# Performance work log

Hardware: AMD Instinct MI355X
Metric: run time of the kernel (lower is better)

## Reference

```python
import jax, jax.numpy as jnp
import numpy as np

N_NODES = 10000
N_EDGES = 640000
IN_CH, HID, OUT_CH = 128, 128, 64


def _gcn_conv(x, edge_index, edge_weight, W, b, n_nodes):
    # PyG GCNConv (default add_self_loops=True, normalize=True, bias=True):
    #   A_hat = A + I ; D = rowsum(A_hat) ; norm_e = D^-1/2[src] * w_e * D^-1/2[dst]
    #   out[dst] += norm_e * (x @ W)[src] ; out += b
    src, dst = edge_index[0], edge_index[1]
    loop = jnp.arange(n_nodes, dtype=edge_index.dtype)
    src = jnp.concatenate([src, loop])
    dst = jnp.concatenate([dst, loop])
    w = jnp.concatenate([edge_weight, jnp.ones((n_nodes,), edge_weight.dtype)])
    deg = jax.ops.segment_sum(w, dst, num_segments=n_nodes)  # scatter on col
    dinv = jnp.where(deg > 0, jax.lax.rsqrt(deg), 0.0).astype(x.dtype)
    norm = dinv[src] * w * dinv[dst]  # [E+N]
    xw = x @ W  # dense GEMM [N, out]
    msg = norm[:, None] * xw[src]  # gather + scale [E+N, out]
    out = jax.ops.segment_sum(msg, dst, num_segments=n_nodes)  # scatter-add
    return out + b


def setup_inputs() -> dict:
    key = jax.random.key(0)
    ks = jax.random.split(key, 8)
    x = jax.random.normal(ks[0], (N_NODES, IN_CH), dtype=jnp.float32)
    edge_index = jax.random.randint(ks[1], (2, N_EDGES), 0, N_NODES, dtype=jnp.int64)
    edge_weight = jax.random.uniform(ks[2], (N_EDGES,), dtype=jnp.float32)
    W1 = jax.random.normal(ks[3], (IN_CH, HID), dtype=jnp.float32) * 0.05
    b1 = jnp.zeros((HID,), jnp.float32)
    W2 = jax.random.normal(ks[4], (HID, OUT_CH), dtype=jnp.float32) * 0.05
    b2 = jnp.zeros((OUT_CH,), jnp.float32)
    return {"x": x, "edge_index": edge_index, "edge_weight": edge_weight,
            "W1": W1, "b1": b1, "W2": W2, "b2": b2}


def reference(x, edge_index, edge_weight, W1, b1, W2, b2):
    h = _gcn_conv(x, edge_index, edge_weight, W1, b1, N_NODES)
    h = jax.nn.relu(h)
    out = _gcn_conv(h, edge_index, edge_weight, W2, b2, N_NODES)
    return out
```

## Files before the change

kernel.cpp:

```cpp
#include <hip/hip_runtime.h>
#include <math.h>

#define N_NODES 10000
#define N_EDGES 640000
#define ELLW    192

#define CHUNKS  64
#define CHUNK_E 10000
#define GB      313

typedef unsigned long long ull;
typedef unsigned int uint;
typedef unsigned short ushort;
typedef unsigned char uchar;

#define FIXED_SCALE 262144.0f


__device__ __forceinline__ float bf_lo(uint u) { return __uint_as_float(u << 16); }
__device__ __forceinline__ float bf_hi(uint u) { return __uint_as_float(u & 0xffff0000u); }
__device__ __forceinline__ ushort f2bf(float v) {
    uint u = __float_as_uint(v);
    uint r = u + 0x7fffu + ((u >> 16) & 1u);
    return (ushort)(r >> 16);
}

__global__ __launch_bounds__(256) void kernelA(const int* __restrict__ ei,
                                               const float* __restrict__ ew,
                                               uint* __restrict__ sd32,
                                               uint* __restrict__ blockcnt,
                                               const float* __restrict__ x,
                                               const float* __restrict__ W1,
                                               ushort* __restrict__ xw1b) {
    __shared__ uint smem[N_NODES];
    const int tid = threadIdx.x;
    if (blockIdx.x < CHUNKS) {
        const int c = blockIdx.x;
        __shared__ int sflag;
        if (tid == 0) sflag = 0;
        for (int i = tid; i < N_NODES; i += 256) smem[i] = 0u;
        __syncthreads();
        int a = (tid < 64) ? ei[2 * (c * CHUNK_E + tid) + 1] : 0;
        if (a) atomicOr(&sflag, 1);
        __syncthreads();
        const int f = sflag;
        const ull* ei64 = (const ull*)ei;
        for (int k = tid; k < CHUNK_E; k += 256) {
            int e = c * CHUNK_E + k;
            int s, d;
            if (f) { s = ei[e];        d = ei[N_EDGES + e]; }
            else   { s = (int)ei64[e]; d = (int)ei64[N_EDGES + e]; }
            float w = ew[e];
            uint fx = (uint)(w * FIXED_SCALE + 0.5f);
            uint old = atomicAdd(&smem[d], (1u << 24) | fx);
            uint r = (old >> 24) & 15u;
            sd32[e] = (r << 28) | ((uint)d << 14) | (uint)s;
        }
        __syncthreads();
        for (int i = tid; i < N_NODES; i += 256)
            blockcnt[c * N_NODES + i] = smem[i];
    } else {
        constexpr int K = 128, TM = 32, KT = 32, NCOL = 128, RPT = 16;
        float* sA = (float*)smem;
        float* sB = sA + TM * (KT + 1);
        int blk = blockIdx.x - CHUNKS;
        int c = tid % NCOL, rr = tid / NCOL;
        int row0 = blk * TM;
        float acc[RPT];
#pragma unroll
        for (int r = 0; r < RPT; ++r) acc[r] = 0.0f;
        for (int k0 = 0; k0 < K; k0 += KT) {
            for (int i = tid; i < TM * KT; i += 256) {
                int r = i / KT, k = i % KT;
                int gr = row0 + r;
                sA[r * (KT + 1) + k] = (gr < N_NODES) ? x[gr * K + k0 + k] : 0.0f;
            }
            for (int i = tid; i < KT * NCOL; i += 256) {
                int k = i / NCOL, cc = i % NCOL;
                sB[k * NCOL + cc] = W1[(k0 + k) * NCOL + cc];
            }
            __syncthreads();
#pragma unroll
            for (int k = 0; k < KT; ++k) {
                float b = sB[k * NCOL + c];
#pragma unroll
                for (int r = 0; r < RPT; ++r)
                    acc[r] += sA[(rr * RPT + r) * (KT + 1) + k] * b;
            }
            __syncthreads();
        }
#pragma unroll
        for (int r = 0; r < RPT; ++r) {
            int gr = row0 + rr * RPT + r;
            if (gr < N_NODES) xw1b[gr * NCOL + c] = f2bf(acc[r]);
        }
    }
}

__global__ __launch_bounds__(256) void scanB(const uint* __restrict__ blockcnt,
                                             uchar* __restrict__ base8,
                                             int* __restrict__ cnt_arr,
                                             float* __restrict__ dinv) {
    int n = blockIdx.x * 256 + threadIdx.x;
    if (n >= N_NODES) return;
    uint wsum = 0;
    int run = 0;
#pragma unroll 8
    for (int c = 0; c < CHUNKS; ++c) {
        uint v = blockcnt[c * N_NODES + n];
        base8[c * N_NODES + n] = (uchar)run;
        run += (int)(v >> 24);
        wsum += v & 0xffffffu;
    }
    cnt_arr[n] = run;
    float dg = 1.0f + (float)wsum * (1.0f / FIXED_SCALE);
    dinv[n] = (float)(1.0 / sqrt((double)dg));
}

__global__ __launch_bounds__(256) void fillC(const uint* __restrict__ sd32,
                                             const float* __restrict__ ew,
                                             const uchar* __restrict__ base8,
                                             const float* __restrict__ dinv,
                                             ull* __restrict__ epack) {
    const int gid = blockIdx.x * 256 + threadIdx.x;
    const int stride = gridDim.x * 256;
    for (int e = gid; e < N_EDGES; e += stride) {
        uint sd = sd32[e];
        int s = (int)(sd & 0x3fffu);
        int d = (int)((sd >> 14) & 0x3fffu);
        int r = (int)(sd >> 28);
        int c = e / CHUNK_E;
        float nrm = dinv[s] * ew[e] * dinv[d];
        int slot = (int)base8[c * N_NODES + d] + r;
        if (slot < ELLW)
            epack[d * ELLW + slot] = ((ull)__float_as_uint(nrm) << 32) | (ull)(uint)s;
    }
}

__global__ __launch_bounds__(256) void aggC(const ushort* __restrict__ xw1b,
                                            const ull* __restrict__ epack,
                                            const int* __restrict__ cnt_arr,
                                            const float* __restrict__ dinv,
                                            const float* __restrict__ b1,
                                            const float* __restrict__ W2,
                                            ushort* __restrict__ xw2b) {
    __shared__ float hl[4][128];
    __shared__ float w2s[128 * 64];
    const uint* __restrict__ xw32 = (const uint*)xw1b;
    const int tid = threadIdx.x;
    int l = tid & 63;
    int wv = tid >> 6;
    int node = blockIdx.x * 4 + wv;

    for (int i = tid; i < 128 * 64; i += 256) w2s[i] = W2[i];

    int cnt = __builtin_amdgcn_readfirstlane(cnt_arr[node]);
    if (cnt > ELLW) cnt = ELLW;
    float dn = dinv[node];
    float d2 = dn * dn;
    uint su = xw32[node * 64 + l];
    float acc0 = d2 * bf_lo(su);
    float acc1 = d2 * bf_hi(su);
    const ull* ep = epack + (long)node * ELLW;
#pragma unroll 8
    for (int j = 0; j < cnt; ++j) {
        ull v = ep[j];
        uint s = (uint)v;
        float n = __uint_as_float((uint)(v >> 32));
        uint u = xw32[s * 64 + l];
        acc0 = fmaf(n, bf_lo(u), acc0);
        acc1 = fmaf(n, bf_hi(u), acc1);
    }
    float2 bb = ((const float2*)b1)[l];
    hl[wv][2 * l]     = fmaxf(acc0 + bb.x, 0.0f);
    hl[wv][2 * l + 1] = fmaxf(acc1 + bb.y, 0.0f);
    __syncthreads();

    float acc = 0.0f;
#pragma unroll 8
    for (int k = 0; k < 128; ++k)
        acc = fmaf(hl[wv][k], w2s[k * 64 + l], acc);
    xw2b[node * 64 + l] = f2bf(acc);
}

__global__ __launch_bounds__(256) void agg2(const ushort* __restrict__ xw2b,
                                            const ull* __restrict__ epack,
                                            const int* __restrict__ cnt_arr,
                                            const float* __restrict__ dinv,
                                            const float* __restrict__ b2,
                                            float* __restrict__ out) {
    const uint* __restrict__ xw32 = (const uint*)xw2b;
    int lane = threadIdx.x & 63;
    int half = lane >> 5;
    int q = lane & 31;
    int pair = blockIdx.x * 4 + (threadIdx.x >> 6);
    int A = pair * 2, B = A + 1;
    int cntA = __builtin_amdgcn_readfirstlane(cnt_arr[A]);
    int cntB = __builtin_amdgcn_readfirstlane(cnt_arr[B]);
    if (cntA > ELLW) cntA = ELLW;
    if (cntB > ELLW) cntB = ELLW;
    int myn = half ? B : A;
    int mycnt = half ? cntB : cntA;
    float dn = dinv[myn];
    float d2 = dn * dn;
    uint su = xw32[myn * 32 + q];
    float acc0 = d2 * bf_lo(su);
    float acc1 = d2 * bf_hi(su);
    const ull* epA = epack + (long)A * ELLW;
    const ull* epB = epack + (long)B * ELLW;
    int mx = cntA > cntB ? cntA : cntB;
#pragma unroll 4
    for (int j = 0; j < mx; ++j) {
        ull vA = epA[j];
        ull vB = epB[j];
        ull v = half ? vB : vA;
        uint s = (uint)v & 0xffffu;
        float n = (j < mycnt) ? __uint_as_float((uint)(v >> 32)) : 0.0f;
        uint u = xw32[s * 32 + q];
        acc0 = fmaf(n, bf_lo(u), acc0);
        acc1 = fmaf(n, bf_hi(u), acc1);
    }
    float2 bb = ((const float2*)b2)[q];
    float2 o;
    o.x = acc0 + bb.x;
    o.y = acc1 + bb.y;
    ((float2*)out)[myn * 32 + q] = o;
}

extern "C" void kernel_launch(void* const* d_in, const int* in_sizes, int n_in,
                              void* d_out, int out_size, void* d_ws, size_t ws_size,
                              hipStream_t stream) {
    const float* x  = (const float*)d_in[0];
    const int*   ei = (const int*)d_in[1];
    const float* ew = (const float*)d_in[2];
    const float* W1 = (const float*)d_in[3];
    const float* b1 = (const float*)d_in[4];
    const float* W2 = (const float*)d_in[5];
    const float* b2 = (const float*)d_in[6];
    float* out = (float*)d_out;

    char* ws = (char*)d_ws;
    ushort* xw1b    = (ushort*)(ws + 0);
    ushort* xw2b    = (ushort*)(ws + 5120000);
    ull*    epack   = (ull*)   (ws + 6400000);
    uint*   blockcnt= (uint*)  (ws + 21760000);
    uchar*  base8   = (uchar*) (ws + 26880000);
    uint*   sd32    = (uint*)  (ws + 28800000);
    int*    cnt_arr = (int*)   (ws + 31360000);
    float*  dinv    = (float*) (ws + 31400000);

    kernelA<<<CHUNKS + GB, 256, 0, stream>>>(ei, ew, sd32, blockcnt, x, W1, xw1b);
    scanB<<<(N_NODES + 255) / 256, 256, 0, stream>>>(blockcnt, base8, cnt_arr, dinv);
    fillC<<<512, 256, 0, stream>>>(sd32, ew, base8, dinv, epack);
    aggC<<<2500, 256, 0, stream>>>(xw1b, epack, cnt_arr, dinv, b1, W2, xw2b);
    agg2<<<1250, 256, 0, stream>>>(xw2b, epack, cnt_arr, dinv, b2, out);
}
```

Measured before the change: 166.4 us.

## Double chunk count, halve GEMM tile rows, and vectorize ELL edge loads

Measured after the change: 162.8 us. 2.2% less time.

```diff
diff --git a/kernel.cpp b/kernel.cpp
--- a/kernel.cpp
+++ b/kernel.cpp
@@ -5,9 +5,9 @@
 #define N_EDGES 640000
 #define ELLW    192
 
-#define CHUNKS  64
-#define CHUNK_E 10000
-#define GB      313
+#define CHUNKS  128
+#define CHUNK_E 5000
+#define GB      625
 
 typedef unsigned long long ull;
 typedef unsigned int uint;
@@ -60,7 +60,7 @@
         for (int i = tid; i < N_NODES; i += 256)
             blockcnt[c * N_NODES + i] = smem[i];
     } else {
-        constexpr int K = 128, TM = 32, KT = 32, NCOL = 128, RPT = 16;
+        constexpr int K = 128, TM = 16, KT = 32, NCOL = 128, RPT = 8;
         float* sA = (float*)smem;
         float* sB = sA + TM * (KT + 1);
         int blk = blockIdx.x - CHUNKS;
@@ -162,8 +162,22 @@
     float acc0 = d2 * bf_lo(su);
     float acc1 = d2 * bf_hi(su);
     const ull* ep = epack + (long)node * ELLW;
-#pragma unroll 8
-    for (int j = 0; j < cnt; ++j) {
+    int j = 0;
+#pragma unroll 4
+    for (; j + 2 <= cnt; j += 2) {
+        ulonglong2 vv = *(const ulonglong2*)(ep + j);
+        uint s0 = (uint)vv.x;
+        float n0 = __uint_as_float((uint)(vv.x >> 32));
+        uint s1 = (uint)vv.y;
+        float n1 = __uint_as_float((uint)(vv.y >> 32));
+        uint u0 = xw32[s0 * 64 + l];
+        uint u1 = xw32[s1 * 64 + l];
+        acc0 = fmaf(n0, bf_lo(u0), acc0);
+        acc1 = fmaf(n0, bf_hi(u0), acc1);
+        acc0 = fmaf(n1, bf_lo(u1), acc0);
+        acc1 = fmaf(n1, bf_hi(u1), acc1);
+    }
+    if (j < cnt) {
         ull v = ep[j];
         uint s = (uint)v;
         float n = __uint_as_float((uint)(v >> 32));
@@ -209,10 +223,26 @@
     const ull* epA = epack + (long)A * ELLW;
     const ull* epB = epack + (long)B * ELLW;
     int mx = cntA > cntB ? cntA : cntB;
+    int j = 0;
 #pragma unroll 4
-    for (int j = 0; j < mx; ++j) {
-        ull vA = epA[j];
-        ull vB = epB[j];
+    for (; j + 2 <= mx; j += 2) {
+        ulonglong2 va = *(const ulonglong2*)(epA + j);
+        ulonglong2 vb = *(const ulonglong2*)(epB + j);
+        ull v0 = half ? vb.x : va.x;
+        ull v1 = half ? vb.y : va.y;
+        uint s0 = (uint)v0 & 0xffffu;
+        float n0 = (j < mycnt) ? __uint_as_float((uint)(v0 >> 32)) : 0.0f;
+        uint s1 = (uint)v1 & 0xffffu;
+        float n1 = (j + 1 < mycnt) ? __uint_as_float((uint)(v1 >> 32)) : 0.0f;
+        uint u0 = xw32[s0 * 32 + q];
+        uint u1 = xw32[s1 * 32 + q];
+        acc0 = fmaf(n0, bf_lo(u0), acc0);
+        acc1 = fmaf(n0, bf_hi(u0), acc1);
+        acc0 = fmaf(n1, bf_lo(u1), acc0);
+        acc1 = fmaf(n1, bf_hi(u1), acc1);
+    }
+    if (j < mx) {
+        ull vA = epA[j], vB = epB[j];
         ull v = half ? vB : vA;
         uint s = (uint)v & 0xffffu;
         float n = (j < mycnt) ? __uint_as_float((uint)(v >> 32)) : 0.0f;
```

## Split per-node edge gathers across waves and double kernelA chunk and tile parallelism

Applied to the files above, without the earlier changes.

Result: no change. 168.4 us (+1.2%).

```diff
diff --git a/kernel.cpp b/kernel.cpp
--- a/kernel.cpp
+++ b/kernel.cpp
@@ -5,9 +5,9 @@
 #define N_EDGES 640000
 #define ELLW    192
 
-#define CHUNKS  64
-#define CHUNK_E 10000
-#define GB      313
+#define CHUNKS  128
+#define CHUNK_E 5000
+#define GB      625
 
 typedef unsigned long long ull;
 typedef unsigned int uint;
@@ -60,7 +60,7 @@
         for (int i = tid; i < N_NODES; i += 256)
             blockcnt[c * N_NODES + i] = smem[i];
     } else {
-        constexpr int K = 128, TM = 32, KT = 32, NCOL = 128, RPT = 16;
+        constexpr int K = 128, TM = 16, KT = 32, NCOL = 128, RPT = 8;
         float* sA = (float*)smem;
         float* sB = sA + TM * (KT + 1);
         int blk = blockIdx.x - CHUNKS;
@@ -137,50 +137,66 @@
     }
 }
 
-__global__ __launch_bounds__(256) void aggC(const ushort* __restrict__ xw1b,
+__global__ __launch_bounds__(512) void aggC(const ushort* __restrict__ xw1b,
                                             const ull* __restrict__ epack,
                                             const int* __restrict__ cnt_arr,
                                             const float* __restrict__ dinv,
                                             const float* __restrict__ b1,
                                             const float* __restrict__ W2,
                                             ushort* __restrict__ xw2b) {
+    __shared__ float part[8][128];
     __shared__ float hl[4][128];
+    __shared__ float sb[128];
     __shared__ float w2s[128 * 64];
     const uint* __restrict__ xw32 = (const uint*)xw1b;
     const int tid = threadIdx.x;
     int l = tid & 63;
     int wv = tid >> 6;
-    int node = blockIdx.x * 4 + wv;
-
-    for (int i = tid; i < 128 * 64; i += 256) w2s[i] = W2[i];
+    int nb = wv >> 1;
+    int halfw = wv & 1;
+    int node = blockIdx.x * 4 + nb;
+
+    for (int i = tid; i < 128 * 64; i += 512) w2s[i] = W2[i];
+    if (tid < 128) sb[tid] = b1[tid];
 
     int cnt = __builtin_amdgcn_readfirstlane(cnt_arr[node]);
     if (cnt > ELLW) cnt = ELLW;
     float dn = dinv[node];
     float d2 = dn * dn;
-    uint su = xw32[node * 64 + l];
-    float acc0 = d2 * bf_lo(su);
-    float acc1 = d2 * bf_hi(su);
+    float acc0, acc1;
+    if (halfw == 0) {
+        uint su = xw32[node * 64 + l];
+        acc0 = d2 * bf_lo(su);
+        acc1 = d2 * bf_hi(su);
+    } else { acc0 = acc1 = 0.0f; }
     const ull* ep = epack + (long)node * ELLW;
-#pragma unroll 8
-    for (int j = 0; j < cnt; ++j) {
+    int iters = (cnt + 1) >> 1;
+#pragma unroll 4
+    for (int i = 0; i < iters; ++i) {
+        int j = 2 * i + halfw;
         ull v = ep[j];
-        uint s = (uint)v;
+        uint s = (uint)v & 0xffffu;
         float n = __uint_as_float((uint)(v >> 32));
+        if (j >= cnt) n = 0.0f;
         uint u = xw32[s * 64 + l];
         acc0 = fmaf(n, bf_lo(u), acc0);
         acc1 = fmaf(n, bf_hi(u), acc1);
     }
-    float2 bb = ((const float2*)b1)[l];
-    hl[wv][2 * l]     = fmaxf(acc0 + bb.x, 0.0f);
-    hl[wv][2 * l + 1] = fmaxf(acc1 + bb.y, 0.0f);
+    part[wv][2 * l]     = acc0;
+    part[wv][2 * l + 1] = acc1;
     __syncthreads();
-
-    float acc = 0.0f;
+    {
+        int nb2 = tid >> 7, k = tid & 127;
+        hl[nb2][k] = fmaxf(part[2 * nb2][k] + part[2 * nb2 + 1][k] + sb[k], 0.0f);
+    }
+    __syncthreads();
+    if (halfw == 0) {
+        float acc = 0.0f;
 #pragma unroll 8
-    for (int k = 0; k < 128; ++k)
-        acc = fmaf(hl[wv][k], w2s[k * 64 + l], acc);
-    xw2b[node * 64 + l] = f2bf(acc);
+        for (int k = 0; k < 128; ++k)
+            acc = fmaf(hl[nb][k], w2s[k * 64 + l], acc);
+        xw2b[node * 64 + l] = f2bf(acc);
+    }
 }
 
 __global__ __launch_bounds__(256) void agg2(const ushort* __restrict__ xw2b,
@@ -191,40 +207,41 @@
                                             float* __restrict__ out) {
     const uint* __restrict__ xw32 = (const uint*)xw2b;
     int lane = threadIdx.x & 63;
-    int half = lane >> 5;
+    int p = lane >> 5;
     int q = lane & 31;
-    int pair = blockIdx.x * 4 + (threadIdx.x >> 6);
-    int A = pair * 2, B = A + 1;
-    int cntA = __builtin_amdgcn_readfirstlane(cnt_arr[A]);
-    int cntB = __builtin_amdgcn_readfirstlane(cnt_arr[B]);
-    if (cntA > ELLW) cntA = ELLW;
-    if (cntB > ELLW) cntB = ELLW;
-    int myn = half ? B : A;
-    int mycnt = half ? cntB : cntA;
-    float dn = dinv[myn];
+    int node = blockIdx.x * 4 + (threadIdx.x >> 6);
+    int cnt = __builtin_amdgcn_readfirstlane(cnt_arr[node]);
+    if (cnt > ELLW) cnt = ELLW;
+    float dn = dinv[node];
     float d2 = dn * dn;
-    uint su = xw32[myn * 32 + q];
-    float acc0 = d2 * bf_lo(su);
-    float acc1 = d2 * bf_hi(su);
-    const ull* epA = epack + (long)A * ELLW;
-    const ull* epB = epack + (long)B * ELLW;
-    int mx = cntA > cntB ? cntA : cntB;
+    float acc0 = 0.0f, acc1 = 0.0f;
+    if (p == 0) {
+        uint su = xw32[node * 32 + q];
+        acc0 = d2 * bf_lo(su);
+        acc1 = d2 * bf_hi(su);
+    }
+    const ull* ep = epack + (long)node * ELLW;
+    int iters = (cnt + 1) >> 1;
 #pragma unroll 4
-    for (int j = 0; j < mx; ++j) {
-        ull vA = epA[j];
-        ull vB = epB[j];
-        ull v = half ? vB : vA;
+    for (int i = 0; i < iters; ++i) {
+        int j = 2 * i + p;
+        ull v = ep[j];
         uint s = (uint)v & 0xffffu;
-        float n = (j < mycnt) ? __uint_as_float((uint)(v >> 32)) : 0.0f;
+        float n = __uint_as_float((uint)(v >> 32));
+        if (j >= cnt) n = 0.0f;
         uint u = xw32[s * 32 + q];
         acc0 = fmaf(n, bf_lo(u), acc0);
         acc1 = fmaf(n, bf_hi(u), acc1);
     }
-    float2 bb = ((const float2*)b2)[q];
-    float2 o;
-    o.x = acc0 + bb.x;
-    o.y = acc1 + bb.y;
-    ((float2*)out)[myn * 32 + q] = o;
+    acc0 += __shfl_xor(acc0, 32);
+    acc1 += __shfl_xor(acc1, 32);
+    if (p == 0) {
+        float2 bb = ((const float2*)b2)[q];
+        float2 o;
+        o.x = acc0 + bb.x;
+        o.y = acc1 + bb.y;
+        ((float2*)out)[node * 32 + q] = o;
+    }
 }
 
 extern "C" void kernel_launch(void* const* d_in, const int* in_sizes, int n_in,
@@ -252,6 +269,6 @@
     kernelA<<<CHUNKS + GB, 256, 0, stream>>>(ei, ew, sd32, blockcnt, x, W1, xw1b);
     scanB<<<(N_NODES + 255) / 256, 256, 0, stream>>>(blockcnt, base8, cnt_arr, dinv);
     fillC<<<512, 256, 0, stream>>>(sd32, ew, base8, dinv, epack);
-    aggC<<<2500, 256, 0, stream>>>(xw1b, epack, cnt_arr, dinv, b1, W2, xw2b);
-    agg2<<<1250, 256, 0, stream>>>(xw2b, epack, cnt_arr, dinv, b2, out);
-}
+    aggC<<<2500, 512, 0, stream>>>(xw1b, epack, cnt_arr, dinv, b1, W2, xw2b);
+    agg2<<<2500, 256, 0, stream>>>(xw2b, epack, cnt_arr, dinv, b2, out);
+}
```
